# Optimization experiments

Hardware: AMD Instinct MI355X
Metric: run time of the kernel (lower is better)

The kernel has to match this reference:

```python
import jax, jax.numpy as jnp
import numpy as np

N = 400000          # residues
A = 15              # padded atoms per residue
BIN_WIDTH = 5.0     # chi_angle_rbf_bin_width
NUM_BINS = int(360.0 / BIN_WIDTH)  # 72
EPS = 1e-6


def setup_inputs() -> dict:
    key = jax.random.key(0)
    ks = jax.random.split(key, 8)
    fixed = jax.random.normal(ks[0], (N, 3, 3), dtype=jnp.float32) * 2.0
    mobile = jax.random.normal(ks[1], (N, 3, 3), dtype=jnp.float32) * 2.0
    coords = jax.random.normal(ks[2], (N, A, 3), dtype=jnp.float32) * 3.0
    prev_atom_coords = jax.random.normal(ks[3], (N, 3, 3), dtype=jnp.float32) * 2.0
    bond_lengths = jax.random.uniform(ks[4], (N, 1), minval=1.2, maxval=1.6, dtype=jnp.float32)
    bond_angles = jax.random.uniform(ks[5], (N, 1), minval=1.6, maxval=2.2, dtype=jnp.float32)
    dihedral_angles = jax.random.uniform(ks[6], (N, 1), minval=-np.pi, maxval=np.pi, dtype=jnp.float32)
    degrees = jax.random.uniform(ks[7], (N, 4), minval=-180.0, maxval=180.0, dtype=jnp.float32)
    return {"fixed": fixed, "mobile": mobile, "coords": coords,
            "prev_atom_coords": prev_atom_coords, "bond_lengths": bond_lengths,
            "bond_angles": bond_angles, "dihedral_angles": dihedral_angles,
            "degrees": degrees}


def _compute_alignment_matrices(fixed, mobile):
    # Kabsch on batched (N,3,3) point triads.
    fixed_com = fixed.mean(axis=1, keepdims=True)      # (N,1,3)
    mob_com = mobile.mean(axis=1, keepdims=True)       # (N,1,3)
    mob_cen = mobile - mob_com
    targ_cen = fixed - fixed_com
    C = jnp.einsum('npi,npj->nij', mob_cen, targ_cen)  # (N,3,3) cross-covariance
    U, _, Wt = jnp.linalg.svd(C)
    R = U @ Wt
    neg_det = jnp.linalg.det(R) < 0.0                  # (N,)
    flip = jnp.asarray([1.0, 1.0, -1.0], dtype=Wt.dtype)[:, None]
    R_fixed = U @ (Wt * flip)                          # flip last row of Wt
    R = jnp.where(neg_det[:, None, None], R_fixed, R)
    return R, mob_com, fixed_com


def _apply_transformation(coords, R, mob_com, fixed_com):
    return (coords - mob_com) @ R + fixed_com


def _extend_coordinates(prev, bond_lengths, bond_angles, dihedral_angles):
    # prev: (N,3,3); angles in radians; returns (N,3)
    bc = prev[:, 1] - prev[:, 2]
    bc = bc / (jnp.linalg.norm(bc, axis=-1, keepdims=True) + EPS)
    ba = jnp.cross(prev[:, 1] - prev[:, 0], bc)
    ba = ba / (jnp.linalg.norm(ba, axis=-1, keepdims=True) + EPS)
    m1 = jnp.cross(ba, bc)
    d1 = bond_lengths * jnp.cos(bond_angles)
    d2 = bond_lengths * jnp.sin(bond_angles) * jnp.cos(dihedral_angles)
    d3 = -bond_lengths * jnp.sin(bond_angles) * jnp.sin(dihedral_angles)
    return prev[:, 2] + bc * d1 + m1 * d2 + ba * d3


def _binned_degree_rbf(degrees):
    # Circular gaussian RBF over [-180,180) with std = bin_width/2.
    std = BIN_WIDTH / 2.0
    centers = jnp.arange(-180.0, 180.0, BIN_WIDTH, dtype=degrees.dtype)  # (72,)
    diff = degrees[..., None] - centers                                   # (N,4,72)
    diff = jnp.mod(diff + 180.0, 360.0) - 180.0                           # circular wrap
    return jnp.exp(-(diff ** 2) / (2.0 * std ** 2))


def reference(fixed, mobile, coords, prev_atom_coords, bond_lengths,
              bond_angles, dihedral_angles, degrees):
    R, mob_com, fixed_com = _compute_alignment_matrices(fixed, mobile)
    aligned = _apply_transformation(coords, R, mob_com, fixed_com)   # (N,A,3)
    next_coords = _extend_coordinates(prev_atom_coords, bond_lengths,
                                      bond_angles, dihedral_angles)  # (N,3)
    chi_embed = _binned_degree_rbf(degrees)                          # (N,4,72)
    return aligned, next_coords, chi_embed
```

## Files before the change

### kernel.cpp

```cpp
#include <hip/hip_runtime.h>
#include <math.h>


typedef float f32x4 __attribute__((ext_vector_type(4)));

__device__ __forceinline__ void kabsch_residue(
    const float* __restrict__ fixed, const float* __restrict__ mobile,
    const float* __restrict__ coords, const float* __restrict__ prev,
    const float* __restrict__ blen, const float* __restrict__ bang,
    const float* __restrict__ dihe,
    float* __restrict__ out_aligned, float* __restrict__ out_next, int n) {
  const float* fp = fixed + (size_t)n * 9;
  const float* mp = mobile + (size_t)n * 9;
  double f[3][3], m[3][3];
#pragma unroll
  for (int p = 0; p < 3; ++p)
#pragma unroll
    for (int i = 0; i < 3; ++i) {
      f[p][i] = (double)fp[p * 3 + i];
      m[p][i] = (double)mp[p * 3 + i];
    }
  double fc[3], mcm[3];
#pragma unroll
  for (int i = 0; i < 3; ++i) {
    fc[i] = (f[0][i] + f[1][i] + f[2][i]) * (1.0 / 3.0);
    mcm[i] = (m[0][i] + m[1][i] + m[2][i]) * (1.0 / 3.0);
  }
  double C[3][3];
#pragma unroll
  for (int i = 0; i < 3; ++i)
#pragma unroll
    for (int j = 0; j < 3; ++j) {
      double s = 0.0;
#pragma unroll
      for (int p = 0; p < 3; ++p) s += (m[p][i] - mcm[i]) * (f[p][j] - fc[j]);
      C[i][j] = s;
    }

  double x01 = C[0][1]*C[1][2] - C[0][2]*C[1][1];
  double y01 = C[0][2]*C[1][0] - C[0][0]*C[1][2];
  double z01 = C[0][0]*C[1][1] - C[0][1]*C[1][0];
  double x02 = C[0][1]*C[2][2] - C[0][2]*C[2][1];
  double y02 = C[0][2]*C[2][0] - C[0][0]*C[2][2];
  double z02 = C[0][0]*C[2][1] - C[0][1]*C[2][0];
  double x12 = C[1][1]*C[2][2] - C[1][2]*C[2][1];
  double y12 = C[1][2]*C[2][0] - C[1][0]*C[2][2];
  double z12 = C[1][0]*C[2][1] - C[1][1]*C[2][0];
  double n01 = x01*x01 + y01*y01 + z01*z01;
  double n02 = x02*x02 + y02*y02 + z02*z02;
  double n12 = x12*x12 + y12*y12 + z12*z12;
  double vx = x01, vy = y01, vz = z01, nn = n01;
  if (n02 > nn) { vx = x02; vy = y02; vz = z02; nn = n02; }
  if (n12 > nn) { vx = x12; vy = y12; vz = z12; nn = n12; }
  double invn = 1.0 / sqrt(fmax(nn, 1e-300));
  vx *= invn; vy *= invn; vz *= invn;

  double av0 = fabs(vx), av1 = fabs(vy), av2 = fabs(vz);
  double w10, w11, w12;
  if (av0 <= av1 && av0 <= av2) {
    w10 = 1.0 - vx*vx; w11 = -vx*vy; w12 = -vx*vz;
  } else if (av1 <= av2) {
    w10 = -vy*vx; w11 = 1.0 - vy*vy; w12 = -vy*vz;
  } else {
    w10 = -vz*vx; w11 = -vz*vy; w12 = 1.0 - vz*vz;
  }
  double iw = 1.0 / sqrt(fmax(w10*w10 + w11*w11 + w12*w12, 1e-300));
  w10 *= iw; w11 *= iw; w12 *= iw;
  double w20 = vy*w12 - vz*w11;
  double w21 = vz*w10 - vx*w12;
  double w22 = vx*w11 - vy*w10;

  double b10 = C[0][0]*w10 + C[0][1]*w11 + C[0][2]*w12;
  double b11 = C[1][0]*w10 + C[1][1]*w11 + C[1][2]*w12;
  double b12 = C[2][0]*w10 + C[2][1]*w11 + C[2][2]*w12;
  double b20 = C[0][0]*w20 + C[0][1]*w21 + C[0][2]*w22;
  double b21 = C[1][0]*w20 + C[1][1]*w21 + C[1][2]*w22;
  double b22 = C[2][0]*w20 + C[2][1]*w21 + C[2][2]*w22;
  double g00 = b10*b10 + b11*b11 + b12*b12;
  double g01 = b10*b20 + b11*b21 + b12*b22;
  double g11 = b20*b20 + b21*b21 + b22*b22;
  double c, s;
  if (fabs(g01) > 1e-300) {
    double tau = (g11 - g00) / (2.0 * g01);
    double tt = 1.0 / (fabs(tau) + sqrt(1.0 + tau * tau));
    if (tau < 0.0) tt = -tt;
    c = 1.0 / sqrt(1.0 + tt * tt);
    s = tt * c;
  } else {
    c = 1.0; s = 0.0;
  }
  double va0 = c*w10 - s*w20, va1 = c*w11 - s*w21, va2 = c*w12 - s*w22;
  double vb0 = s*w10 + c*w20, vb1 = s*w11 + c*w21, vb2 = s*w12 + c*w22;
  double Ca0 = c*b10 - s*b20, Ca1 = c*b11 - s*b21, Ca2 = c*b12 - s*b22;
  double Cb0 = s*b10 + c*b20, Cb1 = s*b11 + c*b21, Cb2 = s*b12 + c*b22;

  double ia = 1.0 / sqrt(fmax(Ca0*Ca0 + Ca1*Ca1 + Ca2*Ca2, 1e-300));
  double ua0 = Ca0 * ia, ua1 = Ca1 * ia, ua2 = Ca2 * ia;
  double pr = ua0*Cb0 + ua1*Cb1 + ua2*Cb2;
  double ub0 = Cb0 - pr*ua0, ub1 = Cb1 - pr*ua1, ub2 = Cb2 - pr*ua2;
  double ib = 1.0 / sqrt(fmax(ub0*ub0 + ub1*ub1 + ub2*ub2, 1e-300));
  ub0 *= ib; ub1 *= ib; ub2 *= ib;
  double uc0 = ua1*ub2 - ua2*ub1;
  double uc1 = ua2*ub0 - ua0*ub2;
  double uc2 = ua0*ub1 - ua1*ub0;
  double vc0 = va1*vb2 - va2*vb1;
  double vc1 = va2*vb0 - va0*vb2;
  double vc2 = va0*vb1 - va1*vb0;
  float r00 = (float)(ua0*va0 + ub0*vb0 + uc0*vc0);
  float r01 = (float)(ua0*va1 + ub0*vb1 + uc0*vc1);
  float r02 = (float)(ua0*va2 + ub0*vb2 + uc0*vc2);
  float r10 = (float)(ua1*va0 + ub1*vb0 + uc1*vc0);
  float r11 = (float)(ua1*va1 + ub1*vb1 + uc1*vc1);
  float r12 = (float)(ua1*va2 + ub1*vb2 + uc1*vc2);
  float r20 = (float)(ua2*va0 + ub2*vb0 + uc2*vc0);
  float r21 = (float)(ua2*va1 + ub2*vb1 + uc2*vc1);
  float r22 = (float)(ua2*va2 + ub2*vb2 + uc2*vc2);
  float mc0 = (float)mcm[0], mc1 = (float)mcm[1], mc2 = (float)mcm[2];
  float fc0 = (float)fc[0], fc1 = (float)fc[1], fc2 = (float)fc[2];

  const float* cb = coords + (size_t)n * 45;
  float* ob = out_aligned + (size_t)n * 45;
#pragma unroll
  for (int a = 0; a < 15; ++a) {
    float x = cb[a * 3 + 0] - mc0;
    float y = cb[a * 3 + 1] - mc1;
    float z = cb[a * 3 + 2] - mc2;
    ob[a * 3 + 0] = x * r00 + y * r10 + z * r20 + fc0;
    ob[a * 3 + 1] = x * r01 + y * r11 + z * r21 + fc1;
    ob[a * 3 + 2] = x * r02 + y * r12 + z * r22 + fc2;
  }

  const float* pp = prev + (size_t)n * 9;
  float p00 = pp[0], p01 = pp[1], p02 = pp[2];
  float p10 = pp[3], p11 = pp[4], p12 = pp[5];
  float p20 = pp[6], p21 = pp[7], p22 = pp[8];
  float bc0 = p10 - p20, bc1 = p11 - p21, bc2 = p12 - p22;
  float nb = sqrtf(bc0*bc0 + bc1*bc1 + bc2*bc2);
  float inb = 1.0f / (nb + 1e-6f);
  bc0 *= inb; bc1 *= inb; bc2 *= inb;
  float e0 = p10 - p00, e1 = p11 - p01, e2 = p12 - p02;
  float ba0 = e1 * bc2 - e2 * bc1;
  float ba1 = e2 * bc0 - e0 * bc2;
  float ba2 = e0 * bc1 - e1 * bc0;
  float nba = sqrtf(ba0*ba0 + ba1*ba1 + ba2*ba2);
  float inba = 1.0f / (nba + 1e-6f);
  ba0 *= inba; ba1 *= inba; ba2 *= inba;
  float m10 = ba1 * bc2 - ba2 * bc1;
  float m11 = ba2 * bc0 - ba0 * bc2;
  float m12 = ba0 * bc1 - ba1 * bc0;
  float L = blen[n], Aa = bang[n], D = dihe[n];
  float sA = sinf(Aa), cA = cosf(Aa), sD = sinf(D), cD = cosf(D);
  float d1 = L * cA;
  float d2 = L * sA * cD;
  float d3 = -L * sA * sD;
  out_next[(size_t)n * 3 + 0] = p20 + bc0 * d1 + m10 * d2 + ba0 * d3;
  out_next[(size_t)n * 3 + 1] = p21 + bc1 * d1 + m11 * d2 + ba1 * d3;
  out_next[(size_t)n * 3 + 2] = p22 + bc2 * d1 + m12 * d2 + ba2 * d3;
}

__global__ __launch_bounds__(256) void rotamer_fused_kernel(
    const float* __restrict__ fixed, const float* __restrict__ mobile,
    const float* __restrict__ coords, const float* __restrict__ prev,
    const float* __restrict__ blen, const float* __restrict__ bang,
    const float* __restrict__ dihe, const float* __restrict__ degrees,
    float* __restrict__ out_aligned, float* __restrict__ out_next,
    f32x4* __restrict__ out_chi, int N, int KB, int total4) {
  int b = blockIdx.x;
  if (b < KB) {
    int n = b * 256 + threadIdx.x;
    if (n < N)
      kabsch_residue(fixed, mobile, coords, prev, blen, bang, dihe,
                     out_aligned, out_next, n);
    return;
  }
  int g = (b - KB) * 256 + threadIdx.x;
  if (g >= total4) return;
  unsigned ug = (unsigned)g;
  unsigned n = ug / 72u;
  unsigned rem = ug - n * 72u;
  unsigned k = rem / 18u;
  unsigned q = rem - k * 18u;
  float deg = degrees[n * 4u + k];
  float base = (float)(q * 20u) - 180.0f;
  f32x4 v;
#pragma unroll
  for (int j = 0; j < 4; ++j) {
    float center = base + 5.0f * (float)j;
    float t = deg - center + 180.0f;
    t = (t < 0.0f) ? t + 360.0f : t;
    t = (t >= 360.0f) ? t - 360.0f : t;
    float dw = t - 180.0f;
    v[j] = __expf(dw * dw * (-1.0f / 12.5f));
  }
  __builtin_nontemporal_store(v, &out_chi[g]);
}

extern "C" void kernel_launch(void* const* d_in, const int* in_sizes, int n_in,
                              void* d_out, int out_size, void* d_ws,
                              size_t ws_size, hipStream_t stream) {
  (void)n_in; (void)d_ws; (void)ws_size; (void)out_size;
  const float* fixed = (const float*)d_in[0];
  const float* mobile = (const float*)d_in[1];
  const float* coords = (const float*)d_in[2];
  const float* prev = (const float*)d_in[3];
  const float* blen = (const float*)d_in[4];
  const float* bang = (const float*)d_in[5];
  const float* dihe = (const float*)d_in[6];
  const float* degrees = (const float*)d_in[7];

  int N = in_sizes[0] / 9;
  float* out = (float*)d_out;
  float* out_aligned = out;
  float* out_next = out + (size_t)N * 45;
  float* out_chi = out + (size_t)N * 48;

  int KB = (N + 255) / 256;
  int total4 = N * 72;
  int CB = (total4 + 255) / 256;
  rotamer_fused_kernel<<<KB + CB, 256, 0, stream>>>(
      fixed, mobile, coords, prev, blen, bang, dihe, degrees,
      out_aligned, out_next, (f32x4*)out_chi, N, KB, total4);
}
```

Before: 130.7 us.

## Stage coords through LDS for coalesced vector loads and stores in Kabsch blocks

Full 256-residue blocks now copy their coords tile into shared memory with coalesced 16-byte loads. Each thread transforms its 45-float slice in place, and the block writes the tile back with coalesced nontemporal vector stores. This replaces the per-thread strided 45-float accesses, which coalesce poorly. In exchange it uses 45KB of LDS per block, which limits occupancy, and adds two block barriers. Per-thread LDS access at a stride of 45 floats may also cause some bank conflicts.

```diff
diff --git a/kernel.cpp b/kernel.cpp
--- a/kernel.cpp
+++ b/kernel.cpp
@@ -4,12 +4,12 @@
 
 typedef float f32x4 __attribute__((ext_vector_type(4)));
 
-__device__ __forceinline__ void kabsch_residue(
-    const float* __restrict__ fixed, const float* __restrict__ mobile,
-    const float* __restrict__ coords, const float* __restrict__ prev,
-    const float* __restrict__ blen, const float* __restrict__ bang,
-    const float* __restrict__ dihe,
-    float* __restrict__ out_aligned, float* __restrict__ out_next, int n) {
+__device__ __forceinline__ void compute_R(
+    const float* __restrict__ fixed, const float* __restrict__ mobile, int n,
+    float& r00, float& r01, float& r02, float& r10, float& r11, float& r12,
+    float& r20, float& r21, float& r22,
+    float& mc0, float& mc1, float& mc2,
+    float& fc0, float& fc1, float& fc2) {
   const float* fp = fixed + (size_t)n * 9;
   const float* mp = mobile + (size_t)n * 9;
   double f[3][3], m[3][3];
@@ -36,7 +36,6 @@
       for (int p = 0; p < 3; ++p) s += (m[p][i] - mcm[i]) * (f[p][j] - fc[j]);
       C[i][j] = s;
     }
-
   double x01 = C[0][1]*C[1][2] - C[0][2]*C[1][1];
   double y01 = C[0][2]*C[1][0] - C[0][0]*C[1][2];
   double z01 = C[0][0]*C[1][1] - C[0][1]*C[1][0];
@@ -54,7 +53,6 @@
   if (n12 > nn) { vx = x12; vy = y12; vz = z12; nn = n12; }
   double invn = 1.0 / sqrt(fmax(nn, 1e-300));
   vx *= invn; vy *= invn; vz *= invn;
-
   double av0 = fabs(vx), av1 = fabs(vy), av2 = fabs(vz);
   double w10, w11, w12;
   if (av0 <= av1 && av0 <= av2) {
@@ -69,7 +67,6 @@
   double w20 = vy*w12 - vz*w11;
   double w21 = vz*w10 - vx*w12;
   double w22 = vx*w11 - vy*w10;
-
   double b10 = C[0][0]*w10 + C[0][1]*w11 + C[0][2]*w12;
   double b11 = C[1][0]*w10 + C[1][1]*w11 + C[1][2]*w12;
   double b12 = C[2][0]*w10 + C[2][1]*w11 + C[2][2]*w12;
@@ -93,7 +90,6 @@
   double vb0 = s*w10 + c*w20, vb1 = s*w11 + c*w21, vb2 = s*w12 + c*w22;
   double Ca0 = c*b10 - s*b20, Ca1 = c*b11 - s*b21, Ca2 = c*b12 - s*b22;
   double Cb0 = s*b10 + c*b20, Cb1 = s*b11 + c*b21, Cb2 = s*b12 + c*b22;
-
   double ia = 1.0 / sqrt(fmax(Ca0*Ca0 + Ca1*Ca1 + Ca2*Ca2, 1e-300));
   double ua0 = Ca0 * ia, ua1 = Ca1 * ia, ua2 = Ca2 * ia;
   double pr = ua0*Cb0 + ua1*Cb1 + ua2*Cb2;
@@ -106,30 +102,23 @@
   double vc0 = va1*vb2 - va2*vb1;
   double vc1 = va2*vb0 - va0*vb2;
   double vc2 = va0*vb1 - va1*vb0;
-  float r00 = (float)(ua0*va0 + ub0*vb0 + uc0*vc0);
-  float r01 = (float)(ua0*va1 + ub0*vb1 + uc0*vc1);
-  float r02 = (float)(ua0*va2 + ub0*vb2 + uc0*vc2);
-  float r10 = (float)(ua1*va0 + ub1*vb0 + uc1*vc0);
-  float r11 = (float)(ua1*va1 + ub1*vb1 + uc1*vc1);
-  float r12 = (float)(ua1*va2 + ub1*vb2 + uc1*vc2);
-  float r20 = (float)(ua2*va0 + ub2*vb0 + uc2*vc0);
-  float r21 = (float)(ua2*va1 + ub2*vb1 + uc2*vc1);
-  float r22 = (float)(ua2*va2 + ub2*vb2 + uc2*vc2);
-  float mc0 = (float)mcm[0], mc1 = (float)mcm[1], mc2 = (float)mcm[2];
-  float fc0 = (float)fc[0], fc1 = (float)fc[1], fc2 = (float)fc[2];
-
-  const float* cb = coords + (size_t)n * 45;
-  float* ob = out_aligned + (size_t)n * 45;
-#pragma unroll
-  for (int a = 0; a < 15; ++a) {
-    float x = cb[a * 3 + 0] - mc0;
-    float y = cb[a * 3 + 1] - mc1;
-    float z = cb[a * 3 + 2] - mc2;
-    ob[a * 3 + 0] = x * r00 + y * r10 + z * r20 + fc0;
-    ob[a * 3 + 1] = x * r01 + y * r11 + z * r21 + fc1;
-    ob[a * 3 + 2] = x * r02 + y * r12 + z * r22 + fc2;
-  }
-
+  r00 = (float)(ua0*va0 + ub0*vb0 + uc0*vc0);
+  r01 = (float)(ua0*va1 + ub0*vb1 + uc0*vc1);
+  r02 = (float)(ua0*va2 + ub0*vb2 + uc0*vc2);
+  r10 = (float)(ua1*va0 + ub1*vb0 + uc1*vc0);
+  r11 = (float)(ua1*va1 + ub1*vb1 + uc1*vc1);
+  r12 = (float)(ua1*va2 + ub1*vb2 + uc1*vc2);
+  r20 = (float)(ua2*va0 + ub2*vb0 + uc2*vc0);
+  r21 = (float)(ua2*va1 + ub2*vb1 + uc2*vc1);
+  r22 = (float)(ua2*va2 + ub2*vb2 + uc2*vc2);
+  mc0 = (float)mcm[0]; mc1 = (float)mcm[1]; mc2 = (float)mcm[2];
+  fc0 = (float)fc[0]; fc1 = (float)fc[1]; fc2 = (float)fc[2];
+}
+
+__device__ __forceinline__ void nerf_next(
+    const float* __restrict__ prev, const float* __restrict__ blen,
+    const float* __restrict__ bang, const float* __restrict__ dihe,
+    float* __restrict__ out_next, int n) {
   const float* pp = prev + (size_t)n * 9;
   float p00 = pp[0], p01 = pp[1], p02 = pp[2];
   float p10 = pp[3], p11 = pp[4], p12 = pp[5];
@@ -158,6 +147,10 @@
   out_next[(size_t)n * 3 + 2] = p22 + bc2 * d1 + m12 * d2 + ba2 * d3;
 }
 
+#define NRES 256
+#define NF (NRES * 45)
+#define NF4 (NF / 4)
+
 __global__ __launch_bounds__(256) void rotamer_fused_kernel(
     const float* __restrict__ fixed, const float* __restrict__ mobile,
     const float* __restrict__ coords, const float* __restrict__ prev,
@@ -167,10 +160,62 @@
     f32x4* __restrict__ out_chi, int N, int KB, int total4) {
   int b = blockIdx.x;
   if (b < KB) {
-    int n = b * 256 + threadIdx.x;
-    if (n < N)
-      kabsch_residue(fixed, mobile, coords, prev, blen, bang, dihe,
-                     out_aligned, out_next, n);
+    __shared__ __attribute__((aligned(16))) float lds[NF];
+    int t = threadIdx.x;
+    int n0 = b * NRES;
+    if (n0 + NRES <= N) {
+      const f32x4* src = (const f32x4*)(coords + (size_t)n0 * 45);
+      f32x4* ldsv = (f32x4*)lds;
+#pragma unroll
+      for (int i = 0; i < 12; ++i) {
+        int idx = i * 256 + t;
+        if (idx < NF4) ldsv[idx] = src[idx];
+      }
+      __syncthreads();
+      int n = n0 + t;
+      float r00, r01, r02, r10, r11, r12, r20, r21, r22;
+      float mc0, mc1, mc2, fc0, fc1, fc2;
+      compute_R(fixed, mobile, n, r00, r01, r02, r10, r11, r12, r20, r21, r22,
+                mc0, mc1, mc2, fc0, fc1, fc2);
+      float* slice = lds + t * 45;
+#pragma unroll
+      for (int a = 0; a < 15; ++a) {
+        float x = slice[a * 3 + 0] - mc0;
+        float y = slice[a * 3 + 1] - mc1;
+        float z = slice[a * 3 + 2] - mc2;
+        slice[a * 3 + 0] = x * r00 + y * r10 + z * r20 + fc0;
+        slice[a * 3 + 1] = x * r01 + y * r11 + z * r21 + fc1;
+        slice[a * 3 + 2] = x * r02 + y * r12 + z * r22 + fc2;
+      }
+      nerf_next(prev, blen, bang, dihe, out_next, n);
+      __syncthreads();
+      f32x4* gout = (f32x4*)(out_aligned + (size_t)n0 * 45);
+#pragma unroll
+      for (int i = 0; i < 12; ++i) {
+        int idx = i * 256 + t;
+        if (idx < NF4) __builtin_nontemporal_store(ldsv[idx], &gout[idx]);
+      }
+    } else {
+      int n = n0 + t;
+      if (n < N) {
+        float r00, r01, r02, r10, r11, r12, r20, r21, r22;
+        float mc0, mc1, mc2, fc0, fc1, fc2;
+        compute_R(fixed, mobile, n, r00, r01, r02, r10, r11, r12, r20, r21,
+                  r22, mc0, mc1, mc2, fc0, fc1, fc2);
+        const float* cb = coords + (size_t)n * 45;
+        float* ob = out_aligned + (size_t)n * 45;
+#pragma unroll
+        for (int a = 0; a < 15; ++a) {
+          float x = cb[a * 3 + 0] - mc0;
+          float y = cb[a * 3 + 1] - mc1;
+          float z = cb[a * 3 + 2] - mc2;
+          ob[a * 3 + 0] = x * r00 + y * r10 + z * r20 + fc0;
+          ob[a * 3 + 1] = x * r01 + y * r11 + z * r21 + fc1;
+          ob[a * 3 + 2] = x * r02 + y * r12 + z * r22 + fc2;
+        }
+        nerf_next(prev, blen, bang, dihe, out_next, n);
+      }
+    }
     return;
   }
   int g = (b - KB) * 256 + threadIdx.x;
@@ -186,10 +231,10 @@
 #pragma unroll
   for (int j = 0; j < 4; ++j) {
     float center = base + 5.0f * (float)j;
-    float t = deg - center + 180.0f;
-    t = (t < 0.0f) ? t + 360.0f : t;
-    t = (t >= 360.0f) ? t - 360.0f : t;
-    float dw = t - 180.0f;
+    float tt = deg - center + 180.0f;
+    tt = (tt < 0.0f) ? tt + 360.0f : tt;
+    tt = (tt >= 360.0f) ? tt - 360.0f : tt;
+    float dw = tt - 180.0f;
     v[j] = __expf(dw * dw * (-1.0f / 12.5f));
   }
   __builtin_nontemporal_store(v, &out_chi[g]);
@@ -214,7 +259,7 @@
   float* out_next = out + (size_t)N * 45;
   float* out_chi = out + (size_t)N * 48;
 
-  int KB = (N + 255) / 256;
+  int KB = (N + NRES - 1) / NRES;
   int total4 = N * 72;
   int CB = (total4 + 255) / 256;
   rotamer_fused_kernel<<<KB + CB, 256, 0, stream>>>(
```

After: 136.0 us. +4.0%, slower.
